# Kernel tuning notes

Measured on AMD Instinct MI355X. Metric: run time of the kernel, lower is better.

Reference implementation:

```python
import jax, jax.numpy as jnp
import numpy as np

N = 20000   # nodes
E = 200000  # directed edges (~kNN k=5, bidirectional)
IN = 256    # in_channels
D = 512     # projected_channels = in_channels * 2
NEG_SLOPE = 0.2


def _ln(x, g, b):
    mu = x.mean(-1, keepdims=True)
    var = ((x - mu) ** 2).mean(-1, keepdims=True)
    return (x - mu) * jax.lax.rsqrt(var + 1e-5) * g + b


def _gat(x, src, dst, W, a_s, a_d, bias, concat):
    # PyG GATConv: linear -> per-edge leaky-relu attention -> segment softmax over dst -> scatter-add
    n = x.shape[0]
    H, C = a_s.shape
    h = (x @ W).reshape(n, H, C)                      # [N,H,C]
    as_n = jnp.einsum('nhc,hc->nh', h, a_s)           # alpha contribution of src node
    ad_n = jnp.einsum('nhc,hc->nh', h, a_d)           # alpha contribution of dst node
    e = jax.nn.leaky_relu(as_n[src] + ad_n[dst], negative_slope=NEG_SLOPE)  # [E,H]
    m = jax.ops.segment_max(e, dst, num_segments=n)   # stable softmax per dst (self-loops => every dst nonempty)
    ex = jnp.exp(e - m[dst])
    den = jax.ops.segment_sum(ex, dst, num_segments=n)
    alpha = ex / den[dst]                             # [E,H]
    out = jax.ops.segment_sum(h[src] * alpha[:, :, None], dst, num_segments=n)  # [N,H,C]
    out = out.reshape(n, H * C) if concat else out.mean(axis=1)
    return out + bias


def setup_inputs() -> dict:
    key = jax.random.key(0)
    ks = jax.random.split(key, 40)
    x = jax.random.normal(ks[0], (N, IN), jnp.float32)
    src = jax.random.randint(ks[1], (E,), 0, N)
    off = jax.random.randint(ks[2], (E,), 1, N)
    dst = (src + off) % N                              # guarantees src != dst
    edge_index = jnp.stack([src, dst]).astype(jnp.int64)

    def p(k, shape, fan):
        return (jax.random.normal(k, shape, jnp.float32) / np.float32(np.sqrt(fan)))

    inp = {
        'x': x, 'edge_index': edge_index,
        'proj_W': p(ks[3], (IN, D), IN), 'proj_b': jnp.zeros((D,), jnp.float32),
        'blk_norm_g': jnp.ones((3, D), jnp.float32), 'blk_norm_b': jnp.zeros((3, D), jnp.float32),
        'g1_W': p(ks[4], (3, D, D), D), 'g1_as': p(ks[5], (3, 4, 128), 128), 'g1_ad': p(ks[6], (3, 4, 128), 128),
        'g1_b': jnp.zeros((3, D), jnp.float32),
        'g2_W': p(ks[7], (3, D, 128), D), 'g2_as': p(ks[8], (3, 2, 64), 64), 'g2_ad': p(ks[9], (3, 2, 64), 64),
        'g2_b': jnp.zeros((3, 128), jnp.float32),
        'uni_W': p(ks[10], (3, 640, D), 640), 'uni_b': jnp.zeros((3, D), jnp.float32),
        'fin_g': jnp.ones((D,), jnp.float32), 'fin_b': jnp.zeros((D,), jnp.float32),
        'fg_W': p(ks[11], (D, 8 * 128), D), 'fg_as': p(ks[12], (8, 128), 128), 'fg_ad': p(ks[13], (8, 128), 128),
        'fg_b': jnp.zeros((128,), jnp.float32),
    }
    return inp


def reference(x, edge_index, proj_W, proj_b, blk_norm_g, blk_norm_b,
              g1_W, g1_as, g1_ad, g1_b, g2_W, g2_as, g2_ad, g2_b,
              uni_W, uni_b, fin_g, fin_b, fg_W, fg_as, fg_ad, fg_b):
    n = x.shape[0]
    loops = jnp.arange(n, dtype=edge_index.dtype)
    src = jnp.concatenate([edge_index[0], loops])     # add_self_loops (PyG default)
    dst = jnp.concatenate([edge_index[1], loops])

    x = jax.nn.elu(x @ proj_W + proj_b)
    for i in range(3):
        res = x
        xn = _ln(x, blk_norm_g[i], blk_norm_b[i])
        o1 = _gat(xn, src, dst, g1_W[i], g1_as[i], g1_ad[i], g1_b[i], True)
        o2 = _gat(xn, src, dst, g2_W[i], g2_as[i], g2_ad[i], g2_b[i], True)
        xc = jax.nn.elu(jnp.concatenate([o1, o2], axis=-1))
        x = res + xc @ uni_W[i] + uni_b[i]
        x = jax.nn.elu(x)
    x = _ln(x, fin_g, fin_b)
    return _gat(x, src, dst, fg_W, fg_as, fg_ad, fg_b, False)  # heads=8, concat=False -> mean
```

## Files before the change

### kernel.cpp

```cpp
#include <hip/hip_runtime.h>
#include <math.h>

#define NN 20000
#define EDGES 200000
#define MPAD 20096

using short8  = __attribute__((ext_vector_type(8))) short;
using short4v = __attribute__((ext_vector_type(4))) short;
using f32x4   = __attribute__((ext_vector_type(4))) float;
typedef unsigned short ushortT;
typedef unsigned int uintT;

__device__ __forceinline__ ushortT f2bfu(float x) {
  union { float f; unsigned u; } c; c.f = x;
  unsigned r = c.u + 0x7FFFu + ((c.u >> 16) & 1u);
  return (ushortT)(r >> 16);
}
__device__ __forceinline__ float bflo(uintT u) {
  union { unsigned i; float f; } c; c.i = u << 16; return c.f;
}
__device__ __forceinline__ float bfhi(uintT u) {
  union { unsigned i; float f; } c; c.i = u & 0xFFFF0000u; return c.f;
}
__device__ __forceinline__ float elu_f(float v) { return v > 0.f ? v : (expf(v) - 1.f); }

__device__ __forceinline__ void acc8(float* acc, uint4 u, float a) {
  acc[0] += a * bflo(u.x); acc[1] += a * bfhi(u.x);
  acc[2] += a * bflo(u.y); acc[3] += a * bfhi(u.y);
  acc[4] += a * bflo(u.z); acc[5] += a * bfhi(u.z);
  acc[6] += a * bflo(u.w); acc[7] += a * bfhi(u.w);
}

__global__ void k_hist(const int* __restrict__ ei, int* __restrict__ cnt) {
  int i = blockIdx.x * 256 + threadIdx.x;
  const int EE = EDGES + NN;
  if (i >= EE) return;
  int d = (i < EDGES) ? ei[EDGES + i] : (i - EDGES);
  atomicAdd(&cnt[d], 1);
}

__global__ __launch_bounds__(256) void k_scan1(const int* __restrict__ cnt,
                                               int* __restrict__ bsum, int n) {
  int b = blockIdx.x, t = threadIdx.x, i = b * 256 + t;
  int v = (i < n) ? cnt[i] : 0;
#pragma unroll
  for (int off = 32; off > 0; off >>= 1) v += __shfl_down(v, off);
  __shared__ int s[4];
  if ((t & 63) == 0) s[t >> 6] = v;
  __syncthreads();
  if (t == 0) bsum[b] = s[0] + s[1] + s[2] + s[3];
}

__global__ void k_scan2(const int* __restrict__ bsum, int* __restrict__ boff,
                        int nb, int* __restrict__ ptr, int n) {
  if (threadIdx.x == 0) {
    int acc = 0;
    for (int b = 0; b < nb; ++b) { boff[b] = acc; acc += bsum[b]; }
    ptr[n] = acc;
  }
}

__global__ __launch_bounds__(256) void k_scan3(const int* __restrict__ cnt,
                                               const int* __restrict__ boff,
                                               int* __restrict__ ptr,
                                               int* __restrict__ cursor, int n) {
  __shared__ int sd[256];
  int b = blockIdx.x, t = threadIdx.x, i = b * 256 + t;
  int v = (i < n) ? cnt[i] : 0;
  sd[t] = v;
  __syncthreads();
  for (int off = 1; off < 256; off <<= 1) {
    int a = (t >= off) ? sd[t - off] : 0;
    __syncthreads();
    sd[t] += a;
    __syncthreads();
  }
  if (i < n) {
    int p = boff[b] + sd[t] - v;
    ptr[i] = p;
    cursor[i] = p;
  }
}

__global__ void k_scatter(const int* __restrict__ ei, int* __restrict__ cursor,
                          int* __restrict__ ssrc) {
  int i = blockIdx.x * 256 + threadIdx.x;
  const int EE = EDGES + NN;
  if (i >= EE) return;
  int s, d;
  if (i < EDGES) { s = ei[i]; d = ei[EDGES + i]; }
  else           { s = i - EDGES; d = s; }
  int pos = atomicAdd(&cursor[d], 1);
  ssrc[pos] = s;
}

struct CvtDesc { const float* src; ushortT* dst; int K; int N; int t0; };
struct CvtArgs { CvtDesc d[11]; };

__global__ __launch_bounds__(256) void k_cvtT(CvtArgs a) {
  __shared__ float tile[32][33];
  int b = blockIdx.x;
  int mi = 0;
#pragma unroll
  for (int i = 1; i < 11; ++i)
    if (b >= a.d[i].t0) mi = i;
  CvtDesc dd = a.d[mi];
  int tb = b - dd.t0;
  int tnc = dd.N / 32;
  int tk = tb / tnc, tn = tb % tnc;
  int t = threadIdx.x;
  {
    int r = t >> 3, c4 = (t & 7) * 4;
    float4 v = *reinterpret_cast<const float4*>(&dd.src[(size_t)(tk * 32 + r) * dd.N + tn * 32 + c4]);
    tile[r][c4 + 0] = v.x; tile[r][c4 + 1] = v.y; tile[r][c4 + 2] = v.z; tile[r][c4 + 3] = v.w;
  }
  __syncthreads();
  {
    int n = t >> 3, k4 = (t & 7) * 4;
    short4v s;
    s.x = (short)f2bfu(tile[k4 + 0][n]);
    s.y = (short)f2bfu(tile[k4 + 1][n]);
    s.z = (short)f2bfu(tile[k4 + 2][n]);
    s.w = (short)f2bfu(tile[k4 + 3][n]);
    *reinterpret_cast<short4v*>(&dd.dst[(size_t)(tn * 32 + n) * dd.K + tk * 32 + k4]) = s;
  }
}

__global__ void k_cvtX(const float* __restrict__ in, ushortT* __restrict__ out, int n4) {
  int i = blockIdx.x * 256 + threadIdx.x;
  if (i >= n4) return;
  float4 v = reinterpret_cast<const float4*>(in)[i];
  short4v s;
  s.x = (short)f2bfu(v.x); s.y = (short)f2bfu(v.y);
  s.z = (short)f2bfu(v.z); s.w = (short)f2bfu(v.w);
  reinterpret_cast<short4v*>(out)[i] = s;
}

__global__ __launch_bounds__(256) void k_ln(const float* __restrict__ in,
                                            const float* __restrict__ g,
                                            const float* __restrict__ b,
                                            ushortT* __restrict__ out) {
  int row = blockIdx.x, t = threadIdx.x;
  const float* r = in + (size_t)row * 512;
  float v0 = r[t], v1 = r[t + 256];
  __shared__ float red[4];
  int w = t >> 6, lane = t & 63;
  float s = v0 + v1;
#pragma unroll
  for (int off = 32; off > 0; off >>= 1) s += __shfl_down(s, off);
  if (lane == 0) red[w] = s;
  __syncthreads();
  float mu = (red[0] + red[1] + red[2] + red[3]) * (1.f / 512.f);
  float d0 = v0 - mu, d1 = v1 - mu;
  float vs = d0 * d0 + d1 * d1;
#pragma unroll
  for (int off = 32; off > 0; off >>= 1) vs += __shfl_down(vs, off);
  __syncthreads();
  if (lane == 0) red[w] = vs;
  __syncthreads();
  float var = (red[0] + red[1] + red[2] + red[3]) * (1.f / 512.f);
  float rs = rsqrtf(var + 1e-5f);
  ushortT* o = out + (size_t)row * 512;
  o[t]       = f2bfu(d0 * rs * g[t]       + b[t]);
  o[t + 256] = f2bfu(d1 * rs * g[t + 256] + b[t + 256]);
}

template <int EPI, bool OUTBF16, int NB>
__global__ __launch_bounds__(256) void k_gemm(const ushortT* __restrict__ A,
                                              const ushortT* __restrict__ Wt,
                                              const float* __restrict__ bias,
                                              const float* __restrict__ res,
                                              void* __restrict__ Outv,
                                              int M, int N, int K) {
  __shared__ short As[128][40];
  __shared__ short Bs[128][40];
  int b = blockIdx.x;
  int x = b & 7, g = b >> 3;
  int mt = x + 8 * (g / NB);
  int nt = g % NB;
  int m0 = mt * 128, n0 = nt * 128;
  if (m0 >= M) return;
  int t = threadIdx.x;
  int w = t >> 6, lane = t & 63;
  int wm = w >> 1, wn = w & 1;
  int lr = lane & 15, lk = (lane >> 4) * 8;
  int sr = t >> 2, sc = (t & 3) * 8;
  int ga0 = m0 + sr, ga1 = m0 + sr + 64;
  const short8 z8 = {};

  short8 vA0, vA1, vB0, vB1;
  {
    vA0 = (ga0 < M) ? *reinterpret_cast<const short8*>(&A[(size_t)ga0 * K + sc]) : z8;
    vA1 = (ga1 < M) ? *reinterpret_cast<const short8*>(&A[(size_t)ga1 * K + sc]) : z8;
    vB0 = *reinterpret_cast<const short8*>(&Wt[(size_t)(n0 + sr) * K + sc]);
    vB1 = *reinterpret_cast<const short8*>(&Wt[(size_t)(n0 + sr + 64) * K + sc]);
  }
  f32x4 acc[4][4] = {};
  for (int k0 = 0; k0 < K; k0 += 32) {
    *reinterpret_cast<short8*>(&As[sr][sc]) = vA0;
    *reinterpret_cast<short8*>(&As[sr + 64][sc]) = vA1;
    *reinterpret_cast<short8*>(&Bs[sr][sc]) = vB0;
    *reinterpret_cast<short8*>(&Bs[sr + 64][sc]) = vB1;
    __syncthreads();
    int k1 = k0 + 32;
    if (k1 < K) {
      vA0 = (ga0 < M) ? *reinterpret_cast<const short8*>(&A[(size_t)ga0 * K + k1 + sc]) : z8;
      vA1 = (ga1 < M) ? *reinterpret_cast<const short8*>(&A[(size_t)ga1 * K + k1 + sc]) : z8;
      vB0 = *reinterpret_cast<const short8*>(&Wt[(size_t)(n0 + sr) * K + k1 + sc]);
      vB1 = *reinterpret_cast<const short8*>(&Wt[(size_t)(n0 + sr + 64) * K + k1 + sc]);
    }
    short8 af[4], bf[4];
#pragma unroll
    for (int m = 0; m < 4; ++m)
      af[m] = *reinterpret_cast<const short8*>(&As[wm * 64 + m * 16 + lr][lk]);
#pragma unroll
    for (int n = 0; n < 4; ++n)
      bf[n] = *reinterpret_cast<const short8*>(&Bs[wn * 64 + n * 16 + lr][lk]);
#pragma unroll
    for (int m = 0; m < 4; ++m)
#pragma unroll
      for (int n = 0; n < 4; ++n)
        acc[m][n] = __builtin_amdgcn_mfma_f32_16x16x32_bf16(af[m], bf[n], acc[m][n], 0, 0, 0);
    __syncthreads();
  }
#pragma unroll
  for (int m = 0; m < 4; ++m) {
#pragma unroll
    for (int n = 0; n < 4; ++n) {
#pragma unroll
      for (int j = 0; j < 4; ++j) {
        int row = wm * 64 + m * 16 + (lane >> 4) * 4 + j;
        int col = wn * 64 + n * 16 + lr;
        int gr = m0 + row, gc = n0 + col;
        if (gr < M) {
          float v = acc[m][n][j];
          if (EPI >= 1) v += bias[gc];
          if (EPI == 2) v += res[(size_t)gr * N + gc];
          if (EPI >= 1) v = elu_f(v);
          if (OUTBF16) ((ushortT*)Outv)[(size_t)gr * N + gc] = f2bfu(v);
          else         ((float*)Outv)[(size_t)gr * N + gc] = v;
        }
      }
    }
  }
}

__global__ __launch_bounds__(384) void k_att_blk(const ushortT* __restrict__ h,
                                                 const float* __restrict__ w1s,
                                                 const float* __restrict__ w1d,
                                                 const float* __restrict__ w2s,
                                                 const float* __restrict__ w2d,
                                                 float* __restrict__ as_n,
                                                 float* __restrict__ ad_n) {
  int n = blockIdx.x;
  int hh = threadIdx.x >> 6, lane = threadIdx.x & 63;
  float s = 0.f, d = 0.f;
  if (hh < 4) {
    int c = lane * 2;
    uintT u = *reinterpret_cast<const uintT*>(&h[(size_t)n * 640 + hh * 128 + c]);
    float lo = bflo(u), hi = bfhi(u);
    s = lo * w1s[hh * 128 + c] + hi * w1s[hh * 128 + c + 1];
    d = lo * w1d[hh * 128 + c] + hi * w1d[hh * 128 + c + 1];
  } else if (lane < 32) {
    int hb = hh - 4;
    int c = lane * 2;
    uintT u = *reinterpret_cast<const uintT*>(&h[(size_t)n * 640 + 512 + hb * 64 + c]);
    float lo = bflo(u), hi = bfhi(u);
    s = lo * w2s[hb * 64 + c] + hi * w2s[hb * 64 + c + 1];
    d = lo * w2d[hb * 64 + c] + hi * w2d[hb * 64 + c + 1];
  }
#pragma unroll
  for (int o = 32; o > 0; o >>= 1) {
    s += __shfl_down(s, o);
    d += __shfl_down(d, o);
  }
  if (lane == 0) {
    as_n[n * 6 + hh] = s;
    ad_n[n * 6 + hh] = d;
  }
}

template <int H, int C>
__global__ void k_att(const ushortT* __restrict__ h, int rs, int off,
                      const float* __restrict__ as_w,
                      const float* __restrict__ ad_w, float* __restrict__ as_n,
                      float* __restrict__ ad_n) {
  int n = blockIdx.x;
  int hh = threadIdx.x >> 6;
  int lane = threadIdx.x & 63;
  float s = 0.f, d = 0.f;
  if (C == 128 || lane < 32) {
    int c = lane * 2;
    uintT u = *reinterpret_cast<const uintT*>(&h[(size_t)n * rs + off + hh * C + c]);
    float lo = bflo(u), hi = bfhi(u);
    s = lo * as_w[hh * C + c] + hi * as_w[hh * C + c + 1];
    d = lo * ad_w[hh * C + c] + hi * ad_w[hh * C + c + 1];
  }
#pragma unroll
  for (int o = 32; o > 0; o >>= 1) {
    s += __shfl_down(s, o);
    d += __shfl_down(d, o);
  }
  if (lane == 0) {
    as_n[n * H + hh] = s;
    ad_n[n * H + hh] = d;
  }
}

template <int H>
__global__ __launch_bounds__(256) void k_soft16(const float* __restrict__ as_n,
                                                const float* __restrict__ ad_n,
                                                const int* __restrict__ rowptr,
                                                const int* __restrict__ ssrc,
                                                float* __restrict__ alpha,
                                                float* __restrict__ rden_out) {
  int t = threadIdx.x;
  int grp16 = t >> 4;
  int l = t & 15;
  int dnode = blockIdx.x * 16 + grp16;
  int e0 = rowptr[dnode], deg = rowptr[dnode + 1] - e0;
  float adv[H], m[H], den[H];
#pragma unroll
  for (int hh = 0; hh < H; ++hh) {
    adv[hh] = ad_n[dnode * H + hh];
    m[hh] = -INFINITY;
    den[hh] = 0.f;
  }
  for (int base = 0; base < deg; base += 16) {
    int j = base + l;
    float e[H];
    if (j < deg) {
      int s = ssrc[e0 + j];
#pragma unroll
      for (int hh = 0; hh < H; ++hh) {
        float v = as_n[s * H + hh] + adv[hh];
        e[hh] = v > 0.f ? v : 0.2f * v;
      }
    } else {
#pragma unroll
      for (int hh = 0; hh < H; ++hh) e[hh] = -INFINITY;
    }
#pragma unroll
    for (int hh = 0; hh < H; ++hh) {
      float v = e[hh];
#pragma unroll
      for (int o = 8; o > 0; o >>= 1) v = fmaxf(v, __shfl_xor(v, o, 16));
      m[hh] = fmaxf(m[hh], v);
    }
  }
  for (int base = 0; base < deg; base += 16) {
    int j = base + l;
    float p[H];
    if (j < deg) {
      int s = ssrc[e0 + j];
#pragma unroll
      for (int hh = 0; hh < H; ++hh) {
        float v = as_n[s * H + hh] + adv[hh];
        v = v > 0.f ? v : 0.2f * v;
        p[hh] = expf(v - m[hh]);
        alpha[(size_t)(e0 + j) * H + hh] = p[hh];
      }
    } else {
#pragma unroll
      for (int hh = 0; hh < H; ++hh) p[hh] = 0.f;
    }
#pragma unroll
    for (int hh = 0; hh < H; ++hh) {
      float v = p[hh];
#pragma unroll
      for (int o = 8; o > 0; o >>= 1) v += __shfl_xor(v, o, 16);
      den[hh] += v;
    }
  }
  if (l == 0) {
#pragma unroll
    for (int hh = 0; hh < H; ++hh)
      rden_out[dnode * H + hh] = 1.f / den[hh];
  }
}

__global__ __launch_bounds__(320) void k_agg_blk(const ushortT* __restrict__ h,
                                                 const float* __restrict__ alpha,
                                                 const float* __restrict__ rden,
                                                 const int* __restrict__ rowptr,
                                                 const int* __restrict__ ssrc,
                                                 const float* __restrict__ b1,
                                                 const float* __restrict__ b2,
                                                 ushortT* __restrict__ out) {
  int dnode = blockIdx.x;
  int t = threadIdx.x;
  int grp = t / 80;
  int r = t - grp * 80;
  int ch0 = r * 8;
  int head = (ch0 < 512) ? (ch0 >> 7) : (4 + ((ch0 - 512) >> 6));
  int e0 = rowptr[dnode], deg = rowptr[dnode + 1] - e0;
  float acc[8] = {};
  __shared__ float s_alpha[64 * 6];
  __shared__ int s_src[64];
  __shared__ float s_part[4][640];
  for (int base = 0; base < deg; base += 64) {
    int cnt = min(64, deg - base);
    __syncthreads();
    for (int tix = t; tix < cnt * 6; tix += 320)
      s_alpha[tix] = alpha[(size_t)(e0 + base) * 6 + tix];
    for (int tix = t; tix < cnt; tix += 320)
      s_src[tix] = ssrc[e0 + base + tix];
    __syncthreads();
    int jj = grp;
    for (; jj + 4 < cnt; jj += 8) {
      int sA = s_src[jj], sB = s_src[jj + 4];
      uint4 uA = *reinterpret_cast<const uint4*>(h + (size_t)sA * 640 + ch0);
      uint4 uB = *reinterpret_cast<const uint4*>(h + (size_t)sB * 640 + ch0);
      acc8(acc, uA, s_alpha[jj * 6 + head]);
      acc8(acc, uB, s_alpha[(jj + 4) * 6 + head]);
    }
    if (jj < cnt) {
      int sA = s_src[jj];
      uint4 uA = *reinterpret_cast<const uint4*>(h + (size_t)sA * 640 + ch0);
      acc8(acc, uA, s_alpha[jj * 6 + head]);
    }
  }
  __syncthreads();
#pragma unroll
  for (int q = 0; q < 8; ++q) s_part[grp][ch0 + q] = acc[q];
  __syncthreads();
  {
    int ch = t * 2;
    int hh = (ch < 512) ? (ch >> 7) : (4 + ((ch - 512) >> 6));
    float rd = rden[dnode * 6 + hh];
    float v0 = s_part[0][ch] + s_part[1][ch] + s_part[2][ch] + s_part[3][ch];
    float v1 = s_part[0][ch + 1] + s_part[1][ch + 1] + s_part[2][ch + 1] + s_part[3][ch + 1];
    v0 *= rd; v1 *= rd;
    v0 += (ch < 512) ? b1[ch] : b2[ch - 512];
    v1 += (ch < 512) ? b1[ch + 1] : b2[ch - 511];
    v0 = elu_f(v0); v1 = elu_f(v1);
    uintT o = (uintT)f2bfu(v0) | ((uintT)f2bfu(v1) << 16);
    *reinterpret_cast<uintT*>(&out[(size_t)dnode * 640 + ch]) = o;
  }
}

__global__ __launch_bounds__(256) void k_agg_mean(
    const ushortT* __restrict__ h, const float* __restrict__ alpha,
    const float* __restrict__ rden,
    const int* __restrict__ rowptr, const int* __restrict__ ssrc,
    const float* __restrict__ bias, float* __restrict__ out) {
  int dnode = blockIdx.x;
  int t = threadIdx.x;
  int grp = t >> 7;
  int r = t & 127;
  int head = r >> 4;
  int e0 = rowptr[dnode], deg = rowptr[dnode + 1] - e0;
  float acc[8] = {};
  __shared__ float s_alpha[64 * 8];
  __shared__ int s_src[64];
  __shared__ float s_part[2][1024];
  for (int base = 0; base < deg; base += 64) {
    int cnt = min(64, deg - base);
    __syncthreads();
    for (int tix = t; tix < cnt * 8; tix += 256)
      s_alpha[tix] = alpha[(size_t)(e0 + base) * 8 + tix];
    for (int tix = t; tix < cnt; tix += 256)
      s_src[tix] = ssrc[e0 + base + tix];
    __syncthreads();
    int jj = grp;
    for (; jj + 2 < cnt; jj += 4) {
      int sA = s_src[jj], sB = s_src[jj + 2];
      uint4 uA = *reinterpret_cast<const uint4*>(h + (size_t)sA * 1024 + r * 8);
      uint4 uB = *reinterpret_cast<const uint4*>(h + (size_t)sB * 1024 + r * 8);
      acc8(acc, uA, s_alpha[jj * 8 + head]);
      acc8(acc, uB, s_alpha[(jj + 2) * 8 + head]);
    }
    if (jj < cnt) {
      int sA = s_src[jj];
      uint4 uA = *reinterpret_cast<const uint4*>(h + (size_t)sA * 1024 + r * 8);
      acc8(acc, uA, s_alpha[jj * 8 + head]);
    }
  }
  __syncthreads();
#pragma unroll
  for (int q = 0; q < 8; ++q) s_part[grp][r * 8 + q] = acc[q];
  __syncthreads();
  if (t < 128) {
    float v = 0.f;
#pragma unroll
    for (int hh = 0; hh < 8; ++hh) {
      float ph = s_part[0][hh * 128 + t] + s_part[1][hh * 128 + t];
      v += ph * rden[dnode * 8 + hh];
    }
    out[(size_t)dnode * 128 + t] = v * 0.125f + bias[t];
  }
}

extern "C" void kernel_launch(void* const* d_in, const int* in_sizes, int n_in,
                              void* d_out, int out_size, void* d_ws, size_t ws_size,
                              hipStream_t stream) {
  const float* x_in   = (const float*)d_in[0];
  const int*   ei     = (const int*)d_in[1];
  const float* proj_W = (const float*)d_in[2];
  const float* proj_b = (const float*)d_in[3];
  const float* bng    = (const float*)d_in[4];
  const float* bnb    = (const float*)d_in[5];
  const float* g1W    = (const float*)d_in[6];
  const float* g1as   = (const float*)d_in[7];
  const float* g1ad   = (const float*)d_in[8];
  const float* g1b    = (const float*)d_in[9];
  const float* g2W    = (const float*)d_in[10];
  const float* g2as   = (const float*)d_in[11];
  const float* g2ad   = (const float*)d_in[12];
  const float* g2b    = (const float*)d_in[13];
  const float* uniW   = (const float*)d_in[14];
  const float* unib   = (const float*)d_in[15];
  const float* fing   = (const float*)d_in[16];
  const float* finb   = (const float*)d_in[17];
  const float* fgW    = (const float*)d_in[18];
  const float* fgas   = (const float*)d_in[19];
  const float* fgad   = (const float*)d_in[20];
  const float* fgb    = (const float*)d_in[21];

  const int EE = EDGES + NN;
  char* ws = (char*)d_ws;
  size_t off = 0;
  auto alloc = [&](size_t bytes) -> void* {
    void* p = ws + off;
    off += (bytes + 255) & ~(size_t)255;
    return p;
  };
  float*   xA    = (float*)alloc((size_t)NN * 512 * 4);
  float*   xB    = (float*)alloc((size_t)NN * 512 * 4);
  ushortT* xn    = (ushortT*)alloc((size_t)MPAD * 512 * 2);
  ushortT* xinb  = (ushortT*)alloc((size_t)MPAD * 256 * 2);
  ushortT* hcat  = (ushortT*)alloc((size_t)NN * 640 * 2);
  ushortT* xc    = (ushortT*)alloc((size_t)MPAD * 640 * 2);
  float*   asb   = (float*)alloc((size_t)NN * 8 * 4);
  float*   adb   = (float*)alloc((size_t)NN * 8 * 4);
  float*   denb  = (float*)alloc((size_t)NN * 8 * 4);
  float*   alphab= (float*)alloc((size_t)EE * 8 * 4);
  ushortT* projT = (ushortT*)alloc((size_t)512 * 256 * 2);
  ushortT* gcatT = (ushortT*)alloc((size_t)3 * 640 * 512 * 2);
  ushortT* uniT  = (ushortT*)alloc((size_t)3 * 512 * 640 * 2);
  ushortT* fgT   = (ushortT*)alloc((size_t)1024 * 512 * 2);
  int* cnt    = (int*)alloc((size_t)NN * 4);
  int* ptr    = (int*)alloc((size_t)(NN + 1) * 4);
  int* cursor = (int*)alloc((size_t)NN * 4);
  int* ssrc   = (int*)alloc((size_t)EE * 4);
  int* bsum   = (int*)alloc((size_t)128 * 4);
  int* boff   = (int*)alloc((size_t)128 * 4);
  ushortT* hf = hcat;

  const int NB79 = (NN + 255) / 256;

  hipMemsetAsync(cnt, 0, (size_t)NN * 4, stream);
  k_hist<<<(EE + 255) / 256, 256, 0, stream>>>(ei, cnt);
  k_scan1<<<NB79, 256, 0, stream>>>(cnt, bsum, NN);
  k_scan2<<<1, 64, 0, stream>>>(bsum, boff, NB79, ptr, NN);
  k_scan3<<<NB79, 256, 0, stream>>>(cnt, boff, ptr, cursor, NN);
  k_scatter<<<(EE + 255) / 256, 256, 0, stream>>>(ei, cursor, ssrc);

  {
    CvtArgs a;
    int t0 = 0;
    auto add = [&](int idx, const float* s, ushortT* d, int K, int N) {
      a.d[idx] = { s, d, K, N, t0 };
      t0 += (K / 32) * (N / 32);
    };
    add(0, proj_W, projT, 256, 512);
    for (int i = 0; i < 3; ++i)
      add(1 + i, g1W + (size_t)i * 512 * 512, gcatT + (size_t)i * 640 * 512, 512, 512);
    for (int i = 0; i < 3; ++i)
      add(4 + i, g2W + (size_t)i * 512 * 128, gcatT + (size_t)i * 640 * 512 + 512 * 512, 512, 128);
    for (int i = 0; i < 3; ++i)
      add(7 + i, uniW + (size_t)i * 640 * 512, uniT + (size_t)i * 512 * 640, 640, 512);
    add(10, fgW, fgT, 512, 1024);
    k_cvtT<<<t0, 256, 0, stream>>>(a);
  }
  k_cvtX<<<(NN * 256 / 4 + 255) / 256, 256, 0, stream>>>(x_in, xinb, NN * 256 / 4);

  const int GMP = 160;

  k_gemm<1, false, 4><<<GMP * 4, 256, 0, stream>>>(xinb, projT, proj_b, nullptr, xA, NN, 512, 256);

  float* cur = xA;
  float* alt = xB;
  for (int i = 0; i < 3; ++i) {
    k_ln<<<NN, 256, 0, stream>>>(cur, bng + i * 512, bnb + i * 512, xn);
    k_gemm<0, true, 5><<<GMP * 5, 256, 0, stream>>>(xn, gcatT + (size_t)i * 640 * 512, nullptr, nullptr, hcat, NN, 640, 512);
    k_att_blk<<<NN, 384, 0, stream>>>(hcat, g1as + i * 512, g1ad + i * 512,
                                      g2as + i * 128, g2ad + i * 128, asb, adb);
    k_soft16<6><<<NN / 16, 256, 0, stream>>>(asb, adb, ptr, ssrc, alphab, denb);
    k_agg_blk<<<NN, 320, 0, stream>>>(hcat, alphab, denb, ptr, ssrc, g1b + i * 512, g2b + i * 128, xc);
    k_gemm<2, false, 4><<<GMP * 4, 256, 0, stream>>>(xc, uniT + (size_t)i * 512 * 640, unib + i * 512, cur, alt, NN, 512, 640);
    float* tmp = cur; cur = alt; alt = tmp;
  }

  k_ln<<<NN, 256, 0, stream>>>(cur, fing, finb, xn);
  k_gemm<0, true, 8><<<GMP * 8, 256, 0, stream>>>(xn, fgT, nullptr, nullptr, hf, NN, 1024, 512);
  k_att<8, 128><<<NN, 512, 0, stream>>>(hf, 1024, 0, fgas, fgad, asb, adb);
  k_soft16<8><<<NN / 16, 256, 0, stream>>>(asb, adb, ptr, ssrc, alphab, denb);
  k_agg_mean<<<NN, 256, 0, stream>>>(hf, alphab, denb, ptr, ssrc, fgb, (float*)d_out);
}
```

Before: 738.6 us.

## Fuse attention logits into GEMM epilogue and softmax into aggregation kernels

Per-node attention logits (src/dst dot products) are now computed in the h-projection GEMM epilogue and accumulated into buffers with atomics. This removes the separate attention kernels that re-read h. The per-destination segment softmax is folded into the aggregation kernels with an online max/sum, so the separate softmax kernel and the per-edge alpha buffer round-trip go away. In exchange there are atomics onto a memset buffer, fp32 logits taken before bf16 rounding, and serial per-head max/exp loops run by only 6–8 threads inside the aggregation blocks.

```diff
diff --git a/kernel.cpp b/kernel.cpp
--- a/kernel.cpp
+++ b/kernel.cpp
@@ -165,12 +165,18 @@
   o[t + 256] = f2bfu(d1 * rs * g[t + 256] + b[t + 256]);
 }
 
-template <int EPI, bool OUTBF16, int NB>
+template <int EPI, bool OUTBF16, int NB, int ATT>
 __global__ __launch_bounds__(256) void k_gemm(const ushortT* __restrict__ A,
                                               const ushortT* __restrict__ Wt,
                                               const float* __restrict__ bias,
                                               const float* __restrict__ res,
                                               void* __restrict__ Outv,
+                                              const float* __restrict__ w1s,
+                                              const float* __restrict__ w1d,
+                                              const float* __restrict__ w2s,
+                                              const float* __restrict__ w2d,
+                                              float* __restrict__ as_out,
+                                              float* __restrict__ ad_out,
                                               int M, int N, int K) {
   __shared__ short As[128][40];
   __shared__ short Bs[128][40];
@@ -243,145 +249,52 @@
       }
     }
   }
-}
-
-__global__ __launch_bounds__(384) void k_att_blk(const ushortT* __restrict__ h,
-                                                 const float* __restrict__ w1s,
-                                                 const float* __restrict__ w1d,
-                                                 const float* __restrict__ w2s,
-                                                 const float* __restrict__ w2d,
-                                                 float* __restrict__ as_n,
-                                                 float* __restrict__ ad_n) {
-  int n = blockIdx.x;
-  int hh = threadIdx.x >> 6, lane = threadIdx.x & 63;
-  float s = 0.f, d = 0.f;
-  if (hh < 4) {
-    int c = lane * 2;
-    uintT u = *reinterpret_cast<const uintT*>(&h[(size_t)n * 640 + hh * 128 + c]);
-    float lo = bflo(u), hi = bfhi(u);
-    s = lo * w1s[hh * 128 + c] + hi * w1s[hh * 128 + c + 1];
-    d = lo * w1d[hh * 128 + c] + hi * w1d[hh * 128 + c + 1];
-  } else if (lane < 32) {
-    int hb = hh - 4;
-    int c = lane * 2;
-    uintT u = *reinterpret_cast<const uintT*>(&h[(size_t)n * 640 + 512 + hb * 64 + c]);
-    float lo = bflo(u), hi = bfhi(u);
-    s = lo * w2s[hb * 64 + c] + hi * w2s[hb * 64 + c + 1];
-    d = lo * w2d[hb * 64 + c] + hi * w2d[hb * 64 + c + 1];
-  }
-#pragma unroll
-  for (int o = 32; o > 0; o >>= 1) {
-    s += __shfl_down(s, o);
-    d += __shfl_down(d, o);
-  }
-  if (lane == 0) {
-    as_n[n * 6 + hh] = s;
-    ad_n[n * 6 + hh] = d;
-  }
-}
-
-template <int H, int C>
-__global__ void k_att(const ushortT* __restrict__ h, int rs, int off,
-                      const float* __restrict__ as_w,
-                      const float* __restrict__ ad_w, float* __restrict__ as_n,
-                      float* __restrict__ ad_n) {
-  int n = blockIdx.x;
-  int hh = threadIdx.x >> 6;
-  int lane = threadIdx.x & 63;
-  float s = 0.f, d = 0.f;
-  if (C == 128 || lane < 32) {
-    int c = lane * 2;
-    uintT u = *reinterpret_cast<const uintT*>(&h[(size_t)n * rs + off + hh * C + c]);
-    float lo = bflo(u), hi = bfhi(u);
-    s = lo * as_w[hh * C + c] + hi * as_w[hh * C + c + 1];
-    d = lo * ad_w[hh * C + c] + hi * ad_w[hh * C + c + 1];
-  }
-#pragma unroll
-  for (int o = 32; o > 0; o >>= 1) {
-    s += __shfl_down(s, o);
-    d += __shfl_down(d, o);
-  }
-  if (lane == 0) {
-    as_n[n * H + hh] = s;
-    ad_n[n * H + hh] = d;
-  }
-}
-
-template <int H>
-__global__ __launch_bounds__(256) void k_soft16(const float* __restrict__ as_n,
-                                                const float* __restrict__ ad_n,
-                                                const int* __restrict__ rowptr,
-                                                const int* __restrict__ ssrc,
-                                                float* __restrict__ alpha,
-                                                float* __restrict__ rden_out) {
-  int t = threadIdx.x;
-  int grp16 = t >> 4;
-  int l = t & 15;
-  int dnode = blockIdx.x * 16 + grp16;
-  int e0 = rowptr[dnode], deg = rowptr[dnode + 1] - e0;
-  float adv[H], m[H], den[H];
-#pragma unroll
-  for (int hh = 0; hh < H; ++hh) {
-    adv[hh] = ad_n[dnode * H + hh];
-    m[hh] = -INFINITY;
-    den[hh] = 0.f;
-  }
-  for (int base = 0; base < deg; base += 16) {
-    int j = base + l;
-    float e[H];
-    if (j < deg) {
-      int s = ssrc[e0 + j];
-#pragma unroll
-      for (int hh = 0; hh < H; ++hh) {
-        float v = as_n[s * H + hh] + adv[hh];
-        e[hh] = v > 0.f ? v : 0.2f * v;
-      }
-    } else {
-#pragma unroll
-      for (int hh = 0; hh < H; ++hh) e[hh] = -INFINITY;
-    }
-#pragma unroll
-    for (int hh = 0; hh < H; ++hh) {
-      float v = e[hh];
-#pragma unroll
-      for (int o = 8; o > 0; o >>= 1) v = fmaxf(v, __shfl_xor(v, o, 16));
-      m[hh] = fmaxf(m[hh], v);
-    }
-  }
-  for (int base = 0; base < deg; base += 16) {
-    int j = base + l;
-    float p[H];
-    if (j < deg) {
-      int s = ssrc[e0 + j];
-#pragma unroll
-      for (int hh = 0; hh < H; ++hh) {
-        float v = as_n[s * H + hh] + adv[hh];
-        v = v > 0.f ? v : 0.2f * v;
-        p[hh] = expf(v - m[hh]);
-        alpha[(size_t)(e0 + j) * H + hh] = p[hh];
-      }
-    } else {
-#pragma unroll
-      for (int hh = 0; hh < H; ++hh) p[hh] = 0.f;
-    }
-#pragma unroll
-    for (int hh = 0; hh < H; ++hh) {
-      float v = p[hh];
-#pragma unroll
-      for (int o = 8; o > 0; o >>= 1) v += __shfl_xor(v, o, 16);
-      den[hh] += v;
-    }
-  }
-  if (l == 0) {
-#pragma unroll
-    for (int hh = 0; hh < H; ++hh)
-      rden_out[dnode * H + hh] = 1.f / den[hh];
+  if (ATT) {
+    float wsv[4], wdv[4];
+#pragma unroll
+    for (int n = 0; n < 4; ++n) {
+      int gc = n0 + wn * 64 + n * 16 + lr;
+      if (ATT == 1) {
+        wsv[n] = (gc < 512) ? w1s[gc] : w2s[gc - 512];
+        wdv[n] = (gc < 512) ? w1d[gc] : w2d[gc - 512];
+      } else {
+        wsv[n] = w1s[gc];
+        wdv[n] = w1d[gc];
+      }
+    }
+    int hc = n0 + wn * 64;
+    int head = (ATT == 1) ? ((hc < 512) ? (hc >> 7) : 4 + ((hc - 512) >> 6))
+                          : (hc >> 7);
+    const int H = (ATT == 1) ? 6 : 8;
+#pragma unroll
+    for (int m = 0; m < 4; ++m) {
+#pragma unroll
+      for (int j = 0; j < 4; ++j) {
+        float sa = 0.f, da = 0.f;
+#pragma unroll
+        for (int n = 0; n < 4; ++n) {
+          float v = acc[m][n][j];
+          sa += v * wsv[n];
+          da += v * wdv[n];
+        }
+#pragma unroll
+        for (int o = 1; o < 16; o <<= 1) {
+          sa += __shfl_xor(sa, o, 16);
+          da += __shfl_xor(da, o, 16);
+        }
+        int gr = m0 + wm * 64 + m * 16 + (lane >> 4) * 4 + j;
+        if (lr == 0 && gr < M) {
+          atomicAdd(&as_out[gr * H + head], sa);
+          atomicAdd(&ad_out[gr * H + head], da);
+        }
+      }
+    }
   }
 }
 
 __global__ __launch_bounds__(320) void k_agg_blk(const ushortT* __restrict__ h,
-                                                 const float* __restrict__ alpha,
-                                                 const float* __restrict__ rden,
+                                                 const float* __restrict__ as_n,
+                                                 const float* __restrict__ ad_n,
                                                  const int* __restrict__ rowptr,
                                                  const int* __restrict__ ssrc,
                                                  const float* __restrict__ b1,
@@ -398,13 +311,55 @@
   __shared__ float s_alpha[64 * 6];
   __shared__ int s_src[64];
   __shared__ float s_part[4][640];
+  __shared__ float s_m[6], s_den[6], s_adv[6];
+  if (t < 6) { s_m[t] = -INFINITY; s_den[t] = 0.f; s_adv[t] = ad_n[dnode * 6 + t]; }
+  __syncthreads();
   for (int base = 0; base < deg; base += 64) {
     int cnt = min(64, deg - base);
-    __syncthreads();
-    for (int tix = t; tix < cnt * 6; tix += 320)
-      s_alpha[tix] = alpha[(size_t)(e0 + base) * 6 + tix];
-    for (int tix = t; tix < cnt; tix += 320)
-      s_src[tix] = ssrc[e0 + base + tix];
+    if (t < cnt) {
+      int s = ssrc[e0 + base + t];
+      s_src[t] = s;
+#pragma unroll
+      for (int hh = 0; hh < 6; ++hh) {
+        float v = as_n[s * 6 + hh] + s_adv[hh];
+        s_alpha[t * 6 + hh] = (v > 0.f) ? v : 0.2f * v;
+      }
+    }
+    __syncthreads();
+    if (t < 6) {
+      float mx = s_m[t];
+      for (int j = 0; j < cnt; ++j) mx = fmaxf(mx, s_alpha[j * 6 + t]);
+      float sc = expf(s_m[t] - mx);
+      float ds = 0.f;
+      for (int j = 0; j < cnt; ++j) ds += expf(s_alpha[j * 6 + t] - mx);
+      s_den[t] = s_den[t] * sc + ds;
+      s_m[t] = mx;
+    }
+    __syncthreads();
+  }
+  if (t < 6) s_den[t] = 1.f / s_den[t];
+  __syncthreads();
+  for (int base = 0; base < deg; base += 64) {
+    int cnt = min(64, deg - base);
+    bool regather = (base > 0) || (deg > 64);
+    if (regather) {
+      __syncthreads();
+      if (t < cnt) {
+        int s = ssrc[e0 + base + t];
+        s_src[t] = s;
+#pragma unroll
+        for (int hh = 0; hh < 6; ++hh) {
+          float v = as_n[s * 6 + hh] + s_adv[hh];
+          s_alpha[t * 6 + hh] = (v > 0.f) ? v : 0.2f * v;
+        }
+      }
+      __syncthreads();
+    }
+    if (t < cnt) {
+#pragma unroll
+      for (int hh = 0; hh < 6; ++hh)
+        s_alpha[t * 6 + hh] = expf(s_alpha[t * 6 + hh] - s_m[hh]) * s_den[hh];
+    }
     __syncthreads();
     int jj = grp;
     for (; jj + 4 < cnt; jj += 8) {
@@ -426,11 +381,8 @@
   __syncthreads();
   {
     int ch = t * 2;
-    int hh = (ch < 512) ? (ch >> 7) : (4 + ((ch - 512) >> 6));
-    float rd = rden[dnode * 6 + hh];
     float v0 = s_part[0][ch] + s_part[1][ch] + s_part[2][ch] + s_part[3][ch];
     float v1 = s_part[0][ch + 1] + s_part[1][ch + 1] + s_part[2][ch + 1] + s_part[3][ch + 1];
-    v0 *= rd; v1 *= rd;
     v0 += (ch < 512) ? b1[ch] : b2[ch - 512];
     v1 += (ch < 512) ? b1[ch + 1] : b2[ch - 511];
     v0 = elu_f(v0); v1 = elu_f(v1);
@@ -440,8 +392,8 @@
 }
 
 __global__ __launch_bounds__(256) void k_agg_mean(
-    const ushortT* __restrict__ h, const float* __restrict__ alpha,
-    const float* __restrict__ rden,
+    const ushortT* __restrict__ h, const float* __restrict__ as_n,
+    const float* __restrict__ ad_n,
     const int* __restrict__ rowptr, const int* __restrict__ ssrc,
     const float* __restrict__ bias, float* __restrict__ out) {
   int dnode = blockIdx.x;
@@ -454,13 +406,55 @@
   __shared__ float s_alpha[64 * 8];
   __shared__ int s_src[64];
   __shared__ float s_part[2][1024];
+  __shared__ float s_m[8], s_den[8], s_adv[8];
+  if (t < 8) { s_m[t] = -INFINITY; s_den[t] = 0.f; s_adv[t] = ad_n[dnode * 8 + t]; }
+  __syncthreads();
   for (int base = 0; base < deg; base += 64) {
     int cnt = min(64, deg - base);
-    __syncthreads();
-    for (int tix = t; tix < cnt * 8; tix += 256)
-      s_alpha[tix] = alpha[(size_t)(e0 + base) * 8 + tix];
-    for (int tix = t; tix < cnt; tix += 256)
-      s_src[tix] = ssrc[e0 + base + tix];
+    if (t < cnt) {
+      int s = ssrc[e0 + base + t];
+      s_src[t] = s;
+#pragma unroll
+      for (int hh = 0; hh < 8; ++hh) {
+        float v = as_n[s * 8 + hh] + s_adv[hh];
+        s_alpha[t * 8 + hh] = (v > 0.f) ? v : 0.2f * v;
+      }
+    }
+    __syncthreads();
+    if (t < 8) {
+      float mx = s_m[t];
+      for (int j = 0; j < cnt; ++j) mx = fmaxf(mx, s_alpha[j * 8 + t]);
+      float sc = expf(s_m[t] - mx);
+      float ds = 0.f;
+      for (int j = 0; j < cnt; ++j) ds += expf(s_alpha[j * 8 + t] - mx);
+      s_den[t] = s_den[t] * sc + ds;
+      s_m[t] = mx;
+    }
+    __syncthreads();
+  }
+  if (t < 8) s_den[t] = 1.f / s_den[t];
+  __syncthreads();
+  for (int base = 0; base < deg; base += 64) {
+    int cnt = min(64, deg - base);
+    bool regather = (base > 0) || (deg > 64);
+    if (regather) {
+      __syncthreads();
+      if (t < cnt) {
+        int s = ssrc[e0 + base + t];
+        s_src[t] = s;
+#pragma unroll
+        for (int hh = 0; hh < 8; ++hh) {
+          float v = as_n[s * 8 + hh] + s_adv[hh];
+          s_alpha[t * 8 + hh] = (v > 0.f) ? v : 0.2f * v;
+        }
+      }
+      __syncthreads();
+    }
+    if (t < cnt) {
+#pragma unroll
+      for (int hh = 0; hh < 8; ++hh)
+        s_alpha[t * 8 + hh] = expf(s_alpha[t * 8 + hh] - s_m[hh]) * s_den[hh];
+    }
     __syncthreads();
     int jj = grp;
     for (; jj + 2 < cnt; jj += 4) {
@@ -483,10 +477,8 @@
   if (t < 128) {
     float v = 0.f;
 #pragma unroll
-    for (int hh = 0; hh < 8; ++hh) {
-      float ph = s_part[0][hh * 128 + t] + s_part[1][hh * 128 + t];
-      v += ph * rden[dnode * 8 + hh];
-    }
+    for (int hh = 0; hh < 8; ++hh)
+      v += s_part[0][hh * 128 + t] + s_part[1][hh * 128 + t];
     out[(size_t)dnode * 128 + t] = v * 0.125f + bias[t];
   }
 }
@@ -533,8 +525,6 @@
   ushortT* xc    = (ushortT*)alloc((size_t)MPAD * 640 * 2);
   float*   asb   = (float*)alloc((size_t)NN * 8 * 4);
   float*   adb   = (float*)alloc((size_t)NN * 8 * 4);
-  float*   denb  = (float*)alloc((size_t)NN * 8 * 4);
-  float*   alphab= (float*)alloc((size_t)EE * 8 * 4);
   ushortT* projT = (ushortT*)alloc((size_t)512 * 256 * 2);
   ushortT* gcatT = (ushortT*)alloc((size_t)3 * 640 * 512 * 2);
   ushortT* uniT  = (ushortT*)alloc((size_t)3 * 512 * 640 * 2);
@@ -577,24 +567,31 @@
 
   const int GMP = 160;
 
-  k_gemm<1, false, 4><<<GMP * 4, 256, 0, stream>>>(xinb, projT, proj_b, nullptr, xA, NN, 512, 256);
+  k_gemm<1, false, 4, 0><<<GMP * 4, 256, 0, stream>>>(
+      xinb, projT, proj_b, nullptr, xA,
+      nullptr, nullptr, nullptr, nullptr, nullptr, nullptr, NN, 512, 256);
 
   float* cur = xA;
   float* alt = xB;
   for (int i = 0; i < 3; ++i) {
     k_ln<<<NN, 256, 0, stream>>>(cur, bng + i * 512, bnb + i * 512, xn);
-    k_gemm<0, true, 5><<<GMP * 5, 256, 0, stream>>>(xn, gcatT + (size_t)i * 640 * 512, nullptr, nullptr, hcat, NN, 640, 512);
-    k_att_blk<<<NN, 384, 0, stream>>>(hcat, g1as + i * 512, g1ad + i * 512,
-                                      g2as + i * 128, g2ad + i * 128, asb, adb);
-    k_soft16<6><<<NN / 16, 256, 0, stream>>>(asb, adb, ptr, ssrc, alphab, denb);
-    k_agg_blk<<<NN, 320, 0, stream>>>(hcat, alphab, denb, ptr, ssrc, g1b + i * 512, g2b + i * 128, xc);
-    k_gemm<2, false, 4><<<GMP * 4, 256, 0, stream>>>(xc, uniT + (size_t)i * 512 * 640, unib + i * 512, cur, alt, NN, 512, 640);
+    hipMemsetAsync(asb, 0, (size_t)2 * NN * 8 * 4, stream);
+    k_gemm<0, true, 5, 1><<<GMP * 5, 256, 0, stream>>>(
+        xn, gcatT + (size_t)i * 640 * 512, nullptr, nullptr, hcat,
+        g1as + i * 512, g1ad + i * 512, g2as + i * 128, g2ad + i * 128,
+        asb, adb, NN, 640, 512);
+    k_agg_blk<<<NN, 320, 0, stream>>>(hcat, asb, adb, ptr, ssrc,
+                                      g1b + i * 512, g2b + i * 128, xc);
+    k_gemm<2, false, 4, 0><<<GMP * 4, 256, 0, stream>>>(
+        xc, uniT + (size_t)i * 512 * 640, unib + i * 512, cur, alt,
+        nullptr, nullptr, nullptr, nullptr, nullptr, nullptr, NN, 512, 640);
     float* tmp = cur; cur = alt; alt = tmp;
   }
 
   k_ln<<<NN, 256, 0, stream>>>(cur, fing, finb, xn);
-  k_gemm<0, true, 8><<<GMP * 8, 256, 0, stream>>>(xn, fgT, nullptr, nullptr, hf, NN, 1024, 512);
-  k_att<8, 128><<<NN, 512, 0, stream>>>(hf, 1024, 0, fgas, fgad, asb, adb);
-  k_soft16<8><<<NN / 16, 256, 0, stream>>>(asb, adb, ptr, ssrc, alphab, denb);
-  k_agg_mean<<<NN, 256, 0, stream>>>(hf, alphab, denb, ptr, ssrc, fgb, (float*)d_out);
-}
+  hipMemsetAsync(asb, 0, (size_t)2 * NN * 8 * 4, stream);
+  k_gemm<0, true, 8, 2><<<GMP * 8, 256, 0, stream>>>(
+      xn, fgT, nullptr, nullptr, hf,
+      fgas, fgad, nullptr, nullptr, asb, adb, NN, 1024, 512);
+  k_agg_mean<<<NN, 256, 0, stream>>>(hf, asb, adb, ptr, ssrc, fgb, (float*)d_out);
+}
```

After: 836.6 us. 1.13x slower.

## Fuse GAT attention-score dot products into GEMM epilogue via atomics

Applied to the files above, without the earlier changes.

Removes the separate per-node attention-score kernels (k_att_blk and k_att). The GEMM that produces h now computes the src and dst attention dot products from its fp32 accumulators. It reduces them across 16 lanes with shuffles and atomically adds partial per-head sums into zeroed buffers. This saves re-reading the large bf16 h matrix and several launches, at the cost of extra epilogue work, a memset per layer and float atomics. The scores are now computed from unrounded fp32 values rather than the stored bf16 h. The memset assumes asb and adb are contiguous.

```diff
diff --git a/kernel.cpp b/kernel.cpp
--- a/kernel.cpp
+++ b/kernel.cpp
@@ -165,12 +165,18 @@
   o[t + 256] = f2bfu(d1 * rs * g[t + 256] + b[t + 256]);
 }
 
-template <int EPI, bool OUTBF16, int NB>
+template <int EPI, bool OUTBF16, int NB, int ATT>
 __global__ __launch_bounds__(256) void k_gemm(const ushortT* __restrict__ A,
                                               const ushortT* __restrict__ Wt,
                                               const float* __restrict__ bias,
                                               const float* __restrict__ res,
                                               void* __restrict__ Outv,
+                                              const float* __restrict__ w1s,
+                                              const float* __restrict__ w1d,
+                                              const float* __restrict__ w2s,
+                                              const float* __restrict__ w2d,
+                                              float* __restrict__ as_out,
+                                              float* __restrict__ ad_out,
                                               int M, int N, int K) {
   __shared__ short As[128][40];
   __shared__ short Bs[128][40];
@@ -243,67 +249,46 @@
       }
     }
   }
-}
-
-__global__ __launch_bounds__(384) void k_att_blk(const ushortT* __restrict__ h,
-                                                 const float* __restrict__ w1s,
-                                                 const float* __restrict__ w1d,
-                                                 const float* __restrict__ w2s,
-                                                 const float* __restrict__ w2d,
-                                                 float* __restrict__ as_n,
-                                                 float* __restrict__ ad_n) {
-  int n = blockIdx.x;
-  int hh = threadIdx.x >> 6, lane = threadIdx.x & 63;
-  float s = 0.f, d = 0.f;
-  if (hh < 4) {
-    int c = lane * 2;
-    uintT u = *reinterpret_cast<const uintT*>(&h[(size_t)n * 640 + hh * 128 + c]);
-    float lo = bflo(u), hi = bfhi(u);
-    s = lo * w1s[hh * 128 + c] + hi * w1s[hh * 128 + c + 1];
-    d = lo * w1d[hh * 128 + c] + hi * w1d[hh * 128 + c + 1];
-  } else if (lane < 32) {
-    int hb = hh - 4;
-    int c = lane * 2;
-    uintT u = *reinterpret_cast<const uintT*>(&h[(size_t)n * 640 + 512 + hb * 64 + c]);
-    float lo = bflo(u), hi = bfhi(u);
-    s = lo * w2s[hb * 64 + c] + hi * w2s[hb * 64 + c + 1];
-    d = lo * w2d[hb * 64 + c] + hi * w2d[hb * 64 + c + 1];
-  }
-#pragma unroll
-  for (int o = 32; o > 0; o >>= 1) {
-    s += __shfl_down(s, o);
-    d += __shfl_down(d, o);
-  }
-  if (lane == 0) {
-    as_n[n * 6 + hh] = s;
-    ad_n[n * 6 + hh] = d;
-  }
-}
-
-template <int H, int C>
-__global__ void k_att(const ushortT* __restrict__ h, int rs, int off,
-                      const float* __restrict__ as_w,
-                      const float* __restrict__ ad_w, float* __restrict__ as_n,
-                      float* __restrict__ ad_n) {
-  int n = blockIdx.x;
-  int hh = threadIdx.x >> 6;
-  int lane = threadIdx.x & 63;
-  float s = 0.f, d = 0.f;
-  if (C == 128 || lane < 32) {
-    int c = lane * 2;
-    uintT u = *reinterpret_cast<const uintT*>(&h[(size_t)n * rs + off + hh * C + c]);
-    float lo = bflo(u), hi = bfhi(u);
-    s = lo * as_w[hh * C + c] + hi * as_w[hh * C + c + 1];
-    d = lo * ad_w[hh * C + c] + hi * ad_w[hh * C + c + 1];
-  }
-#pragma unroll
-  for (int o = 32; o > 0; o >>= 1) {
-    s += __shfl_down(s, o);
-    d += __shfl_down(d, o);
-  }
-  if (lane == 0) {
-    as_n[n * H + hh] = s;
-    ad_n[n * H + hh] = d;
+  if (ATT) {
+    float wsv[4], wdv[4];
+#pragma unroll
+    for (int n = 0; n < 4; ++n) {
+      int gc = n0 + wn * 64 + n * 16 + lr;
+      if (ATT == 1) {
+        wsv[n] = (gc < 512) ? w1s[gc] : w2s[gc - 512];
+        wdv[n] = (gc < 512) ? w1d[gc] : w2d[gc - 512];
+      } else {
+        wsv[n] = w1s[gc];
+        wdv[n] = w1d[gc];
+      }
+    }
+    int hc = n0 + wn * 64;
+    int head = (ATT == 1) ? ((hc < 512) ? (hc >> 7) : 4 + ((hc - 512) >> 6))
+                          : (hc >> 7);
+    const int H = (ATT == 1) ? 6 : 8;
+#pragma unroll
+    for (int m = 0; m < 4; ++m) {
+#pragma unroll
+      for (int j = 0; j < 4; ++j) {
+        float sa = 0.f, da = 0.f;
+#pragma unroll
+        for (int n = 0; n < 4; ++n) {
+          float v = acc[m][n][j];
+          sa += v * wsv[n];
+          da += v * wdv[n];
+        }
+#pragma unroll
+        for (int o = 1; o < 16; o <<= 1) {
+          sa += __shfl_xor(sa, o, 16);
+          da += __shfl_xor(da, o, 16);
+        }
+        int gr = m0 + wm * 64 + m * 16 + (lane >> 4) * 4 + j;
+        if (lr == 0 && gr < M) {
+          atomicAdd(&as_out[gr * H + head], sa);
+          atomicAdd(&ad_out[gr * H + head], da);
+        }
+      }
+    }
   }
 }
 
@@ -577,24 +562,33 @@
 
   const int GMP = 160;
 
-  k_gemm<1, false, 4><<<GMP * 4, 256, 0, stream>>>(xinb, projT, proj_b, nullptr, xA, NN, 512, 256);
+  k_gemm<1, false, 4, 0><<<GMP * 4, 256, 0, stream>>>(
+      xinb, projT, proj_b, nullptr, xA,
+      nullptr, nullptr, nullptr, nullptr, nullptr, nullptr, NN, 512, 256);
 
   float* cur = xA;
   float* alt = xB;
   for (int i = 0; i < 3; ++i) {
     k_ln<<<NN, 256, 0, stream>>>(cur, bng + i * 512, bnb + i * 512, xn);
-    k_gemm<0, true, 5><<<GMP * 5, 256, 0, stream>>>(xn, gcatT + (size_t)i * 640 * 512, nullptr, nullptr, hcat, NN, 640, 512);
-    k_att_blk<<<NN, 384, 0, stream>>>(hcat, g1as + i * 512, g1ad + i * 512,
-                                      g2as + i * 128, g2ad + i * 128, asb, adb);
+    hipMemsetAsync(asb, 0, (size_t)2 * NN * 8 * 4, stream);
+    k_gemm<0, true, 5, 1><<<GMP * 5, 256, 0, stream>>>(
+        xn, gcatT + (size_t)i * 640 * 512, nullptr, nullptr, hcat,
+        g1as + i * 512, g1ad + i * 512, g2as + i * 128, g2ad + i * 128,
+        asb, adb, NN, 640, 512);
     k_soft16<6><<<NN / 16, 256, 0, stream>>>(asb, adb, ptr, ssrc, alphab, denb);
-    k_agg_blk<<<NN, 320, 0, stream>>>(hcat, alphab, denb, ptr, ssrc, g1b + i * 512, g2b + i * 128, xc);
-    k_gemm<2, false, 4><<<GMP * 4, 256, 0, stream>>>(xc, uniT + (size_t)i * 512 * 640, unib + i * 512, cur, alt, NN, 512, 640);
+    k_agg_blk<<<NN, 320, 0, stream>>>(hcat, alphab, denb, ptr, ssrc,
+                                      g1b + i * 512, g2b + i * 128, xc);
+    k_gemm<2, false, 4, 0><<<GMP * 4, 256, 0, stream>>>(
+        xc, uniT + (size_t)i * 512 * 640, unib + i * 512, cur, alt,
+        nullptr, nullptr, nullptr, nullptr, nullptr, nullptr, NN, 512, 640);
     float* tmp = cur; cur = alt; alt = tmp;
   }
 
   k_ln<<<NN, 256, 0, stream>>>(cur, fing, finb, xn);
-  k_gemm<0, true, 8><<<GMP * 8, 256, 0, stream>>>(xn, fgT, nullptr, nullptr, hf, NN, 1024, 512);
-  k_att<8, 128><<<NN, 512, 0, stream>>>(hf, 1024, 0, fgas, fgad, asb, adb);
+  hipMemsetAsync(asb, 0, (size_t)2 * NN * 8 * 4, stream);
+  k_gemm<0, true, 8, 2><<<GMP * 8, 256, 0, stream>>>(
+      xn, fgT, nullptr, nullptr, hf,
+      fgas, fgad, nullptr, nullptr, asb, adb, NN, 1024, 512);
   k_soft16<8><<<NN / 16, 256, 0, stream>>>(asb, adb, ptr, ssrc, alphab, denb);
   k_agg_mean<<<NN, 256, 0, stream>>>(hf, alphab, denb, ptr, ssrc, fgb, (float*)d_out);
 }
```

Result: slower. 758.8 us (+2.7%).
